# Kernel optimization log

Measured on AMD Instinct MI355X. Metric: run time of the kernel, lower is better.

Reference implementation:

```python
import jax, jax.numpy as jnp
import numpy as np

N, E, F, H, R, NB, G, C = 100000, 500000, 128, 64, 16, 30, 1000, 10


def setup_inputs() -> dict:
    key = jax.random.key(0)
    ks = jax.random.split(key, 12)
    s = 0.05
    x = jax.random.normal(ks[0], (N, F), jnp.float32)
    edge_index = jax.random.randint(ks[1], (2, E), 0, N, dtype=jnp.int32)
    edge_norm = jax.random.uniform(ks[2], (E,), jnp.float32)
    edge_type = jax.random.randint(ks[3], (E,), 0, R, dtype=jnp.int32)
    seq_lengths = jnp.full((G,), N // G, dtype=jnp.int32)  # 1000 graphs x 100 nodes
    return dict(
        x=x, edge_index=edge_index, edge_norm=edge_norm, edge_type=edge_type,
        seq_lengths=seq_lengths, avec=0,
        w1_rel=jax.random.normal(ks[4], (F, H), jnp.float32) * s,
        w1_root=jax.random.normal(ks[5], (F, H), jnp.float32) * s,
        b1=jnp.zeros((H,), jnp.float32),
        bases=jax.random.normal(ks[6], (NB, H, H), jnp.float32) * s,
        comp=jax.random.normal(ks[7], (R, NB), jnp.float32) * s,
        w2_root=jax.random.normal(ks[8], (H, H), jnp.float32) * s,
        b2=jnp.zeros((H,), jnp.float32),
        lin_w=jax.random.normal(ks[9], (2 * (F + H), H), jnp.float32) * s,
        lin_b=jnp.zeros((H,), jnp.float32),
        fc_w=jax.random.normal(ks[10], (H, C), jnp.float32) * s,
        fc_b=jnp.zeros((C,), jnp.float32),
    )


def reference(x, edge_index, edge_norm, edge_type, seq_lengths, avec,
              w1_rel, w1_root, b1, bases, comp, w2_root, b2,
              lin_w, lin_b, fc_w, fc_b):
    src, dst = edge_index[0], edge_index[1]

    # --- GraphConv (PyG): out_i = W_rel @ sum_{j->i} w_ji x_j + W_root x_i + b
    msg = x[src] * edge_norm[:, None]                       # [E, F]
    agg = jax.ops.segment_sum(msg, dst, num_segments=N)     # [N, F]
    h = agg @ w1_rel + x @ w1_root + b1                     # [N, H]

    # --- RGCNConv with basis decomposition, mean aggregation per relation
    W = jnp.einsum('rb,bio->rio', comp, bases)              # [R, H, H]
    hs = h[src]                                             # [E, H]
    out = h @ w2_root + b2                                  # root transform + bias
    for r in range(R):  # small fixed relation count
        m = (edge_type == r).astype(h.dtype)                # [E]
        s_r = jax.ops.segment_sum(hs * m[:, None], dst, num_segments=N)
        c_r = jax.ops.segment_sum(m, dst, num_segments=N)
        out = out + (s_r / jnp.maximum(c_r, 1.0)[:, None]) @ W[r]

    feats = jnp.concatenate([x, out], axis=-1)              # [N, F+H]

    # --- ragged per-graph sum & max pooling (replaces the Python loop)
    bounds = jnp.cumsum(seq_lengths)
    gid = jnp.searchsorted(bounds, jnp.arange(N), side='right')  # [N] graph ids
    gsum = jax.ops.segment_sum(feats, gid, num_segments=G)       # [G, F+H]
    gmax = jax.ops.segment_max(feats, gid, num_segments=G)       # [G, F+H]

    hidden = jax.nn.relu(jnp.concatenate([gsum, gmax], -1) @ lin_w + lin_b)
    # dropout is identity at inference
    logits = hidden @ fc_w + fc_b                           # [G, C]
    if avec:
        return logits
    return jax.nn.log_softmax(logits, -1)
```

## Files before the change

### kernel.cpp

```cpp
#include <hip/hip_runtime.h>
#include <hip/hip_bf16.h>

#define NN 100000
#define NE 500000
#define FD 128
#define HD 64
#define RR 16
#define NBASE 30
#define GG 1000
#define CC 10
#define NGROUP 6250
#define NBLK ((NE + 255) / 256)
#define NDBLK ((NN + 256) / 256)


typedef __attribute__((ext_vector_type(8))) short bf16x8;
typedef __attribute__((ext_vector_type(4))) float f32x4;

__device__ inline unsigned short f2b(float x) {
  __hip_bfloat16 b = __float2bfloat16(x);
  return *reinterpret_cast<unsigned short*>(&b);
}
__device__ inline float b2f(unsigned short u) {
  return __uint_as_float(((unsigned)u) << 16);
}
__device__ inline unsigned pk2(float a, float b) {
  return (unsigned)f2b(a) | ((unsigned)f2b(b) << 16);
}

__global__ void k_prep(const float* comp, const float* bases, const float* w_root,
                       const float* w_rel, const float* w2, unsigned short* Wt,
                       unsigned short* wcat2, unsigned short* w2t, int* hist2) {
  int bx = blockIdx.x;
  if (bx < 256) {
    int idx = bx * 256 + threadIdx.x;
    int r = idx >> 12, kj = idx & 4095;
    int k = kj >> 6, n = kj & 63;
    float acc = 0.0f;
    for (int b = 0; b < NBASE; ++b)
      acc += comp[r * NBASE + b] * bases[b * 4096 + kj];
    int sk = (k & 15) * 4 + (k >> 4);
    Wt[(r << 12) + n * 64 + sk] = f2b(acc);
  } else if (bx < 336) {
    int idx = (bx - 256) * 256 + threadIdx.x;
    if (idx < 16384) {
      int n = idx >> 7, k = idx & 127;
      float v = (n < 64) ? w_root[k * 64 + n] : w_rel[k * 64 + (n - 64)];
      int nt = n >> 4, m = n & 15;
      int s = k >> 5, q = (k >> 3) & 3, j = k & 7;
      wcat2[(((nt * 4 + s) * 64) + q * 16 + m) * 8 + j] = f2b(v);
    } else if (idx < 16384 + 4096) {
      int i2 = idx - 16384;
      int n = i2 >> 6, k = i2 & 63;
      int sk = (k & 15) * 4 + (k >> 4);
      w2t[n * 64 + sk] = f2b(w2[k * 64 + n]);
    }
  } else {
    int idx = (bx - 336) * 1024 + threadIdx.x * 4;
    if (idx < NN * RR)
      *reinterpret_cast<int4*>(hist2 + idx) = make_int4(0, 0, 0, 0);
  }
}

__global__ __launch_bounds__(256) void k_proj_mfma(const float* x, const unsigned short* wcat2,
                                                   const float* b1, unsigned short* hroot_bf,
                                                   unsigned short* xw_bf) {
  __shared__ unsigned short wsh[16384];
  int wv = threadIdx.x >> 6, l = threadIdx.x & 63, m = l & 15, q = l >> 4;
  int g = blockIdx.x * 4 + wv;
  int gc = (g < NGROUP) ? g : (NGROUP - 1);
  size_t n0 = (size_t)gc * 16;
  const float* xr = x + (n0 + m) * FD + q * 8;
  float4 xv[8];
#pragma unroll
  for (int s = 0; s < 4; ++s) {
    xv[2 * s] = *reinterpret_cast<const float4*>(xr + s * 32);
    xv[2 * s + 1] = *reinterpret_cast<const float4*>(xr + s * 32 + 4);
  }
  {
    const uint4* wsrc = reinterpret_cast<const uint4*>(wcat2);
    uint4* wdst = reinterpret_cast<uint4*>(wsh);
#pragma unroll
    for (int r = 0; r < 8; ++r)
      wdst[r * 256 + threadIdx.x] = wsrc[r * 256 + threadIdx.x];
  }
  __syncthreads();
  if (g >= NGROUP) return;
  bf16x8 afr[4];
#pragma unroll
  for (int s = 0; s < 4; ++s) {
    float4 xa = xv[2 * s], xb = xv[2 * s + 1];
    bf16x8 a;
    a[0] = (short)f2b(xa.x); a[1] = (short)f2b(xa.y);
    a[2] = (short)f2b(xa.z); a[3] = (short)f2b(xa.w);
    a[4] = (short)f2b(xb.x); a[5] = (short)f2b(xb.y);
    a[6] = (short)f2b(xb.z); a[7] = (short)f2b(xb.w);
    afr[s] = a;
  }
  f32x4 acc[8];
#pragma unroll
  for (int nt = 0; nt < 8; ++nt) acc[nt] = (f32x4){0, 0, 0, 0};
#pragma unroll
  for (int s = 0; s < 4; ++s) {
#pragma unroll
    for (int nt = 0; nt < 8; ++nt) {
      bf16x8 b = *reinterpret_cast<const bf16x8*>(wsh + (size_t)((nt * 4 + s) * 64 + l) * 8);
      acc[nt] = __builtin_amdgcn_mfma_f32_16x16x32_bf16(afr[s], b, acc[nt], 0, 0, 0);
    }
  }
  float bv[4];
#pragma unroll
  for (int nt = 0; nt < 4; ++nt) bv[nt] = b1[nt * 16 + m];
#pragma unroll
  for (int i = 0; i < 4; ++i) {
    size_t row = (n0 + q * 4 + i) * 64 + m * 4;
    uint2 oh, ox;
    oh.x = pk2(acc[0][i] + bv[0], acc[1][i] + bv[1]);
    oh.y = pk2(acc[2][i] + bv[2], acc[3][i] + bv[3]);
    ox.x = pk2(acc[4][i], acc[5][i]);
    ox.y = pk2(acc[6][i], acc[7][i]);
    *reinterpret_cast<uint2*>(hroot_bf + row) = oh;
    *reinterpret_cast<uint2*>(xw_bf + row) = ox;
  }
}

__global__ void k_hists(const int* ei, const int* etype, int* bch, int* hist2) {
  __shared__ int lh[RR];
  if (threadIdx.x < RR) lh[threadIdx.x] = 0;
  __syncthreads();
  int e = blockIdx.x * 256 + threadIdx.x;
  if (e < NE) {
    int t = etype[e];
    atomicAdd(&lh[t], 1);
    atomicAdd(&hist2[ei[NE + e] * RR + t], 1);
  }
  __syncthreads();
  if (threadIdx.x < RR) bch[blockIdx.x * RR + threadIdx.x] = lh[threadIdx.x];
}

__device__ inline int block_scan_incl(int v, int* ps, int t) {
  ps[t] = v;
  __syncthreads();
  for (int off = 1; off < 256; off <<= 1) {
    int u = (t >= off) ? ps[t - off] : 0;
    __syncthreads();
    ps[t] += u;
    __syncthreads();
  }
  return ps[t];
}

__device__ inline int dst_degree(const int* hist2, int dst) {
  const int4* hp = reinterpret_cast<const int4*>(hist2 + dst * RR);
  int4 a = hp[0], b = hp[1], c = hp[2], d = hp[3];
  return a.x + a.y + a.z + a.w + b.x + b.y + b.z + b.w +
         c.x + c.y + c.z + c.w + d.x + d.y + d.z + d.w;
}

__global__ void k_scanA(const int* hist2, int* bsum) {
  __shared__ int red[256];
  int t = threadIdx.x;
  int dst = blockIdx.x * 256 + t;
  red[t] = (dst < NN) ? dst_degree(hist2, dst) : 0;
  __syncthreads();
  for (int s = 128; s; s >>= 1) {
    if (t < s) red[t] += red[t + s];
    __syncthreads();
  }
  if (t == 0) bsum[blockIdx.x] = red[0];
}

__global__ void k_scanC(const int* hist2, const int* bsum, int* rowptr_d, int* ctr_d) {
  int t = threadIdx.x;
  int dst = blockIdx.x * 256 + t;
  int v = (dst < NN) ? dst_degree(hist2, dst) : 0;
  __shared__ int ps[256];
  int incl = block_scan_incl(v, ps, t);
  int ex = bsum[blockIdx.x] + incl - v;
  if (dst <= NN) { rowptr_d[dst] = ex; ctr_d[dst] = ex; }
}

__global__ void k_bscan(const int* bch, const int* seq, int* bsum, int* bbase,
                        int* offs, int* bounds) {
  __shared__ int part[16][17], chunkbase[16][17];
  __shared__ int colbase[16];
  __shared__ int ps[256];
  int t = threadIdx.x;
  {
    int i0 = t * 2, i1 = t * 2 + 1;
    int l0 = (i0 < NDBLK) ? bsum[i0] : 0;
    int l1 = (i1 < NDBLK) ? bsum[i1] : 0;
    int sa = l0 + l1;
    int incla = block_scan_incl(sa, ps, t);
    int run = incla - sa;
    if (i0 < NDBLK) bsum[i0] = run;
    run += l0;
    if (i1 < NDBLK) bsum[i1] = run;
  }
  __syncthreads();
  int ty = t & 15, ck = t >> 4;
  const int CH = (NBLK + 15) / 16;
  int b0 = ck * CH, b1 = min(b0 + CH, NBLK);
  int s = 0;
  for (int b = b0; b < b1; ++b) s += bch[b * 16 + ty];
  part[ck][ty] = s;
  __syncthreads();
  if (t < 16) {
    int run = 0;
    for (int c = 0; c < 16; ++c) { chunkbase[c][t] = run; run += part[c][t]; }
    colbase[t] = run;
  }
  __syncthreads();
  if (t == 0) {
    int run = 0;
    for (int r = 0; r < RR; ++r) { int v = colbase[r]; offs[r] = run; colbase[r] = run; run += v; }
    offs[RR] = run;
  }
  __syncthreads();
  {
    int run = colbase[ty] + chunkbase[ck][ty];
    for (int b = b0; b < b1; ++b) {
      int v = bch[b * 16 + ty];
      bbase[b * 16 + ty] = run;
      run += v;
    }
  }
  __syncthreads();
  int loc[4];
  int ss = 0;
  if (t < 250) {
    for (int i = 0; i < 4; ++i) { loc[i] = seq[t * 4 + i]; ss += loc[i]; }
  }
  int incl = block_scan_incl(ss, ps, t);
  int base = incl - ss;
  if (t < 250) {
    int run = base;
    for (int i = 0; i < 4; ++i) { run += loc[i]; bounds[t * 4 + i] = run; }
  }
}

__global__ void k_sort(const int* ei, const int* etype, const float* enorm,
                       const int* bbase, const int* hist2, int* ctr_d,
                       uint4* tse, uint2* esen) {
  __shared__ int lcnt[RR];
  if (threadIdx.x < RR) lcnt[threadIdx.x] = 0;
  __syncthreads();
  int e = blockIdx.x * 256 + threadIdx.x;
  if (e >= NE) return;
  int t = etype[e];
  int rank = atomicAdd(&lcnt[t], 1);
  int p = bbase[blockIdx.x * RR + t] + rank;
  int src = ei[e];
  int dst = ei[NE + e];
  int cnt = hist2[dst * RR + t];
  float inv = 1.0f / (float)max(cnt, 1);
  int pos = atomicAdd(&ctr_d[dst], 1);
  esen[pos] = make_uint2((unsigned)src, __float_as_uint(enorm[e]));
  tse[p] = make_uint4((unsigned)src, __float_as_uint(inv), (unsigned)pos, 0u);
}

__global__ __launch_bounds__(256) void k_gconv_seg(const int* rowptr_d, const uint2* esen,
    const unsigned short* xw_bf, const unsigned short* hroot_bf, unsigned short* h_bf) {
  int wv = threadIdx.x >> 6, l = threadIdx.x & 63;
  int c4 = l & 15, eq = l >> 4;
  int dst = blockIdx.x * 4 + wv;
  int lo = rowptr_d[dst];
  int hi = rowptr_d[dst + 1];
  float4 acc = {0.0f, 0.0f, 0.0f, 0.0f};
  for (int base0 = lo; base0 < hi; base0 += 64) {
    int n = min(64, hi - base0);
    int sv = 0;
    float nv = 0.0f;
    if (l < n) {
      uint2 se = esen[base0 + l];
      sv = (int)se.x;
      nv = __uint_as_float(se.y);
    }
    int k4max = (n + 3) >> 2;
    for (int k4 = 0; k4 < k4max; ++k4) {
      int eid = k4 * 4 + eq;
      int s = __shfl(sv, eid);
      float w = __shfl(nv, eid);
      if (eid < n) {
        uint2 v = *reinterpret_cast<const uint2*>(xw_bf + (size_t)s * 64 + c4 * 4);
        acc.x += b2f((unsigned short)(v.x & 0xffffu)) * w;
        acc.y += b2f((unsigned short)(v.x >> 16)) * w;
        acc.z += b2f((unsigned short)(v.y & 0xffffu)) * w;
        acc.w += b2f((unsigned short)(v.y >> 16)) * w;
      }
    }
  }
  acc.x += __shfl_xor(acc.x, 16); acc.y += __shfl_xor(acc.y, 16);
  acc.z += __shfl_xor(acc.z, 16); acc.w += __shfl_xor(acc.w, 16);
  acc.x += __shfl_xor(acc.x, 32); acc.y += __shfl_xor(acc.y, 32);
  acc.z += __shfl_xor(acc.z, 32); acc.w += __shfl_xor(acc.w, 32);
  if (l < 16) {
    uint2 hb = *reinterpret_cast<const uint2*>(hroot_bf + (size_t)dst * 64 + l * 4);
    acc.x += b2f((unsigned short)(hb.x & 0xffffu));
    acc.y += b2f((unsigned short)(hb.x >> 16));
    acc.z += b2f((unsigned short)(hb.y & 0xffffu));
    acc.w += b2f((unsigned short)(hb.y >> 16));
    uint2 o;
    o.x = pk2(acc.x, acc.y);
    o.y = pk2(acc.z, acc.w);
    *reinterpret_cast<uint2*>(h_bf + (size_t)dst * 64 + l * 4) = o;
  }
}

__global__ __launch_bounds__(256) void k_rgcn_y(const uint4* tse, const int* offs,
    const unsigned short* h_bf, const unsigned short* Wt, unsigned short* y_bf) {
  int r = blockIdx.x;
  int lo = offs[r], hi = offs[r + 1];
  int cnt = hi - lo;
  int wv = threadIdx.x >> 6;
  int l = threadIdx.x & 63;
  int m = l & 15, q = l >> 4;
  int ngroups = (cnt + 15) / 16;
  const unsigned short* Wr = Wt + (r << 12);
  bf16x8 bfr[2][4];
#pragma unroll
  for (int s = 0; s < 2; ++s)
#pragma unroll
    for (int nt = 0; nt < 4; ++nt)
      bfr[s][nt] = *reinterpret_cast<const bf16x8*>(Wr + (nt * 16 + m) * 64 + s * 32 + q * 8);

  for (int g = blockIdx.y * 4 + wv; g < ngroups; g += gridDim.y * 4) {
    int base = lo + g * 16;
    int ne = min(16, hi - base);
    int p = base + ((m < ne) ? m : 0);
    uint4 t4 = tse[p];
    int src = (int)t4.x;
    float inv = __uint_as_float(t4.y);
    int pos = (int)t4.z;
    f32x4 acc[4];
#pragma unroll
    for (int nt = 0; nt < 4; ++nt) acc[nt] = (f32x4){0, 0, 0, 0};
    const unsigned short* hrow = h_bf + (size_t)src * 64 + q * 8;
#pragma unroll
    for (int s = 0; s < 2; ++s) {
      bf16x8 afr = *reinterpret_cast<const bf16x8*>(hrow + s * 32);
#pragma unroll
      for (int nt = 0; nt < 4; ++nt)
        acc[nt] = __builtin_amdgcn_mfma_f32_16x16x32_bf16(afr, bfr[s][nt], acc[nt], 0, 0, 0);
    }
#pragma unroll
    for (int i = 0; i < 4; ++i) {
      int row = q * 4 + i;
      float ir = __shfl(inv, row);
      int pr = __shfl(pos, row);
      if (row < ne) {
        uint2 o;
        o.x = pk2(acc[0][i] * ir, acc[1][i] * ir);
        o.y = pk2(acc[2][i] * ir, acc[3][i] * ir);
        *reinterpret_cast<uint2*>(y_bf + (size_t)pr * 64 + m * 4) = o;
      }
    }
  }
}

__global__ __launch_bounds__(256) void k_out(const int* rowptr_d, const unsigned short* y_bf,
    const unsigned short* h_bf, const unsigned short* w2t, const float* b2, float* out) {
  __shared__ float ldsC[16][68];
  int wv = threadIdx.x >> 6, l = threadIdx.x & 63;
  int c4 = l & 15, eq = l >> 4;
  size_t d0 = (size_t)blockIdx.x * 16;
  for (int dd = 0; dd < 4; ++dd) {
    int dst = (int)d0 + wv * 4 + dd;
    int lo = rowptr_d[dst];
    int hi = rowptr_d[dst + 1];
    float4 acc = {0.0f, 0.0f, 0.0f, 0.0f};
    for (int row = lo + eq; row < hi; row += 4) {
      uint2 v = *reinterpret_cast<const uint2*>(y_bf + (size_t)row * 64 + c4 * 4);
      acc.x += b2f((unsigned short)(v.x & 0xffffu));
      acc.y += b2f((unsigned short)(v.x >> 16));
      acc.z += b2f((unsigned short)(v.y & 0xffffu));
      acc.w += b2f((unsigned short)(v.y >> 16));
    }
    acc.x += __shfl_xor(acc.x, 16); acc.y += __shfl_xor(acc.y, 16);
    acc.z += __shfl_xor(acc.z, 16); acc.w += __shfl_xor(acc.w, 16);
    acc.x += __shfl_xor(acc.x, 32); acc.y += __shfl_xor(acc.y, 32);
    acc.z += __shfl_xor(acc.z, 32); acc.w += __shfl_xor(acc.w, 32);
    if (l < 16)
      *reinterpret_cast<float4*>(&ldsC[wv * 4 + dd][l * 4]) = acc;
  }
  __syncthreads();
  int m = l & 15, q = l >> 4, nt = wv;
  float bb = b2[nt * 16 + m];
  f32x4 acc;
#pragma unroll
  for (int i = 0; i < 4; ++i) acc[i] = ldsC[q * 4 + i][m * 4 + nt] + bb;
#pragma unroll
  for (int s = 0; s < 2; ++s) {
    bf16x8 a = *reinterpret_cast<const bf16x8*>(h_bf + (d0 + m) * 64 + s * 32 + q * 8);
    bf16x8 b = *reinterpret_cast<const bf16x8*>(w2t + (nt * 16 + m) * 64 + s * 32 + q * 8);
    acc = __builtin_amdgcn_mfma_f32_16x16x32_bf16(a, b, acc, 0, 0, 0);
  }
#pragma unroll
  for (int i = 0; i < 4; ++i)
    out[(d0 + q * 4 + i) * 64 + nt * 16 + m] = acc[i];
}

__global__ __launch_bounds__(256) void k_head(const float* x, const float* outn,
    const int* bounds, const float* lin_w, const float* lin_b,
    const float* fc_w, const float* fc_b, float* dout) {
  __shared__ float4 psum[5][48], pmax[5][48];
  __shared__ float gsum[192], gmax[192];
  __shared__ float part[4][64];
  __shared__ float hid[HD], lg[CC], mred[2];
  int g = blockIdx.x, t = threadIdx.x;
  int lo = (g == 0) ? 0 : bounds[g - 1];
  int hi = bounds[g];
  int nn = hi - lo;
  if (t < 240) {
    int c4 = t % 48, ch = t / 48;
    int a = lo + (nn * ch) / 5, b = lo + (nn * (ch + 1)) / 5;
    float4 s = {0, 0, 0, 0};
    float4 mx = {-3.4e38f, -3.4e38f, -3.4e38f, -3.4e38f};
    const float* bp;
    int stride;
    if (c4 < 32) { bp = x + (size_t)a * FD + c4 * 4; stride = FD; }
    else         { bp = outn + (size_t)a * 64 + (c4 - 32) * 4; stride = 64; }
    int n = a;
    for (; n + 4 <= b; n += 4) {
      float4 v0 = *reinterpret_cast<const float4*>(bp);
      float4 v1 = *reinterpret_cast<const float4*>(bp + stride);
      float4 v2 = *reinterpret_cast<const float4*>(bp + 2 * stride);
      float4 v3 = *reinterpret_cast<const float4*>(bp + 3 * stride);
      bp += 4 * stride;
      s.x += v0.x + v1.x + v2.x + v3.x;
      s.y += v0.y + v1.y + v2.y + v3.y;
      s.z += v0.z + v1.z + v2.z + v3.z;
      s.w += v0.w + v1.w + v2.w + v3.w;
      mx.x = fmaxf(fmaxf(fmaxf(mx.x, v0.x), fmaxf(v1.x, v2.x)), v3.x);
      mx.y = fmaxf(fmaxf(fmaxf(mx.y, v0.y), fmaxf(v1.y, v2.y)), v3.y);
      mx.z = fmaxf(fmaxf(fmaxf(mx.z, v0.z), fmaxf(v1.z, v2.z)), v3.z);
      mx.w = fmaxf(fmaxf(fmaxf(mx.w, v0.w), fmaxf(v1.w, v2.w)), v3.w);
    }
    for (; n < b; ++n) {
      float4 v = *reinterpret_cast<const float4*>(bp);
      bp += stride;
      s.x += v.x; s.y += v.y; s.z += v.z; s.w += v.w;
      mx.x = fmaxf(mx.x, v.x); mx.y = fmaxf(mx.y, v.y);
      mx.z = fmaxf(mx.z, v.z); mx.w = fmaxf(mx.w, v.w);
    }
    psum[ch][c4] = s;
    pmax[ch][c4] = mx;
  }
  __syncthreads();
  if (t < 48) {
    float4 s = psum[0][t], m = pmax[0][t];
#pragma unroll
    for (int ch = 1; ch < 5; ++ch) {
      float4 ps = psum[ch][t], pm = pmax[ch][t];
      s.x += ps.x; s.y += ps.y; s.z += ps.z; s.w += ps.w;
      m.x = fmaxf(m.x, pm.x); m.y = fmaxf(m.y, pm.y);
      m.z = fmaxf(m.z, pm.z); m.w = fmaxf(m.w, pm.w);
    }
    gsum[t * 4 + 0] = s.x; gsum[t * 4 + 1] = s.y;
    gsum[t * 4 + 2] = s.z; gsum[t * 4 + 3] = s.w;
    gmax[t * 4 + 0] = m.x; gmax[t * 4 + 1] = m.y;
    gmax[t * 4 + 2] = m.z; gmax[t * 4 + 3] = m.w;
  }
  __syncthreads();
  {
    int o = t & 63, pp = t >> 6;
    float a = 0.0f;
    int k0 = pp * 96;
    for (int k = k0; k < k0 + 96; ++k) {
      float gv = (k < 192) ? gsum[k] : gmax[k - 192];
      a += gv * lin_w[k * 64 + o];
    }
    part[pp][o] = a;
  }
  __syncthreads();
  if (t < HD) {
    float a = lin_b[t] + part[0][t] + part[1][t] + part[2][t] + part[3][t];
    hid[t] = fmaxf(a, 0.0f);
  }
  __syncthreads();
  if (t < CC) {
    float a = fc_b[t];
    for (int k = 0; k < HD; ++k) a += hid[k] * fc_w[k * CC + t];
    lg[t] = a;
  }
  __syncthreads();
  if (t == 0) {
    float mm = lg[0];
#pragma unroll
    for (int i = 1; i < CC; ++i) mm = fmaxf(mm, lg[i]);
    float se = 0.0f;
#pragma unroll
    for (int i = 0; i < CC; ++i) se += __expf(lg[i] - mm);
    mred[0] = mm;
    mred[1] = __logf(se);
  }
  __syncthreads();
  if (t < CC) dout[g * CC + t] = lg[t] - mred[0] - mred[1];
}

extern "C" void kernel_launch(void* const* d_in, const int* in_sizes, int n_in,
                              void* d_out, int out_size, void* d_ws, size_t ws_size,
                              hipStream_t stream) {
  const float* x     = (const float*)d_in[0];
  const int* ei      = (const int*)d_in[1];
  const float* enorm = (const float*)d_in[2];
  const int* etype   = (const int*)d_in[3];
  const int* seq     = (const int*)d_in[4];
  const float* w1_rel  = (const float*)d_in[6];
  const float* w1_root = (const float*)d_in[7];
  const float* b1      = (const float*)d_in[8];
  const float* bases   = (const float*)d_in[9];
  const float* comp    = (const float*)d_in[10];
  const float* w2      = (const float*)d_in[11];
  const float* b2      = (const float*)d_in[12];
  const float* lin_w   = (const float*)d_in[13];
  const float* lin_b   = (const float*)d_in[14];
  const float* fc_w    = (const float*)d_in[15];
  const float* fc_b    = (const float*)d_in[16];
  float* dout = (float*)d_out;

  char* p = (char*)d_ws;
  unsigned short* hroot_bf = (unsigned short*)p; p += (size_t)NN * 64 * 2;
  unsigned short* xw_bf    = (unsigned short*)p; p += (size_t)NN * 64 * 2;
  float* out  = (float*)p;  p += (size_t)NN * 64 * 4;
  unsigned short* y_bf = (unsigned short*)p; p += (size_t)NE * 64 * 2;
  unsigned short* h_bf = (unsigned short*)p; p += (size_t)NN * 64 * 2;
  unsigned short* Wt   = (unsigned short*)p; p += (size_t)RR * 4096 * 2;
  unsigned short* wcat2 = (unsigned short*)p; p += (size_t)128 * 128 * 2;
  unsigned short* w2t  = (unsigned short*)p; p += (size_t)64 * 64 * 2;
  uint4* tse   = (uint4*)p; p += (size_t)NE * 16;
  uint2* esen  = (uint2*)p; p += (size_t)NE * 8;
  int* hist2   = (int*)p; p += (size_t)NN * RR * 4;
  int* rowptr_d = (int*)p; p += (size_t)(NDBLK * 256) * 4;
  int* bch     = (int*)p; p += (size_t)NBLK * RR * 4;
  int* bbase   = (int*)p; p += (size_t)NBLK * RR * 4;
  int* bsum    = (int*)p; p += (size_t)NGROUP * 4;
  int* offs    = (int*)p; p += 68;
  int* bounds  = (int*)p; p += (size_t)GG * 4;
  int* ctr_d   = (int*)out;

  const int ZBLK = (NN * RR + 1023) / 1024;
  hipLaunchKernelGGL(k_prep, dim3(336 + ZBLK), dim3(256), 0, stream,
                     comp, bases, w1_root, w1_rel, w2, Wt, wcat2, w2t, hist2);
  hipLaunchKernelGGL(k_proj_mfma, dim3((NGROUP + 3) / 4), dim3(256), 0, stream,
                     x, wcat2, b1, hroot_bf, xw_bf);
  hipLaunchKernelGGL(k_hists, dim3(NBLK), dim3(256), 0, stream, ei, etype, bch, hist2);
  hipLaunchKernelGGL(k_scanA, dim3(NDBLK), dim3(256), 0, stream, hist2, bsum);
  hipLaunchKernelGGL(k_bscan, dim3(1), dim3(256), 0, stream, bch, seq, bsum, bbase, offs, bounds);
  hipLaunchKernelGGL(k_scanC, dim3(NDBLK), dim3(256), 0, stream, hist2, bsum, rowptr_d, ctr_d);
  hipLaunchKernelGGL(k_sort, dim3(NBLK), dim3(256), 0, stream,
                     ei, etype, enorm, bbase, hist2, ctr_d, tse, esen);
  hipLaunchKernelGGL(k_gconv_seg, dim3(NN / 4), dim3(256), 0, stream,
                     rowptr_d, esen, xw_bf, hroot_bf, h_bf);
  hipLaunchKernelGGL(k_rgcn_y, dim3(RR, 128), dim3(256), 0, stream,
                     tse, offs, h_bf, Wt, y_bf);
  hipLaunchKernelGGL(k_out, dim3(NN / 16), dim3(256), 0, stream,
                     rowptr_d, y_bf, h_bf, w2t, b2, out);
  hipLaunchKernelGGL(k_head, dim3(GG), dim3(256), 0, stream, x, out, bounds,
                     lin_w, lin_b, fc_w, fc_b, dout);
}
```

Baseline: 331.1 us.

## Fuse per-graph sum/max pooling of RGCN output into k_out via atomics

k_out no longer writes the full per-node output; it reduces each 4-row fragment and atomically adds into per-graph sums and atomically maxes into order-preserving uint keys. k_head then only pools the x features and reads the pre-pooled RGCN part. This removes a large intermediate write and read, at the cost of global atomics and a binary search for graph ids in k_out. The zeroed workspace is extended to cover the new accumulators, and the counter buffer gets its own allocation.

```diff
diff --git a/kernel.cpp b/kernel.cpp
--- a/kernel.cpp
+++ b/kernel.cpp
@@ -12,6 +12,8 @@
 #define NGROUP 6250
 #define NBLK ((NE + 255) / 256)
 #define NDBLK ((NN + 256) / 256)
+#define TOTZ (NN * RR + GG * HD * 2)
+#define ZBLK ((TOTZ + 1023) / 1024)
 
 
 typedef __attribute__((ext_vector_type(8))) short bf16x8;
@@ -27,10 +29,18 @@
 __device__ inline unsigned pk2(float a, float b) {
   return (unsigned)f2b(a) | ((unsigned)f2b(b) << 16);
 }
+__device__ inline unsigned fkey(float f) {
+  unsigned b = __float_as_uint(f);
+  return (b & 0x80000000u) ? ~b : (b | 0x80000000u);
+}
+__device__ inline float fdec(unsigned k) {
+  unsigned b = (k & 0x80000000u) ? (k & 0x7FFFFFFFu) : ~k;
+  return __uint_as_float(b);
+}
 
 __global__ void k_prep(const float* comp, const float* bases, const float* w_root,
                        const float* w_rel, const float* w2, unsigned short* Wt,
-                       unsigned short* wcat2, unsigned short* w2t, int* hist2) {
+                       unsigned short* wcat2, unsigned short* w2t, int* zbase) {
   int bx = blockIdx.x;
   if (bx < 256) {
     int idx = bx * 256 + threadIdx.x;
@@ -57,8 +67,8 @@
     }
   } else {
     int idx = (bx - 336) * 1024 + threadIdx.x * 4;
-    if (idx < NN * RR)
-      *reinterpret_cast<int4*>(hist2 + idx) = make_int4(0, 0, 0, 0);
+    if (idx < TOTZ)
+      *reinterpret_cast<int4*>(zbase + idx) = make_int4(0, 0, 0, 0);
   }
 }
 
@@ -359,11 +369,22 @@
 }
 
 __global__ __launch_bounds__(256) void k_out(const int* rowptr_d, const unsigned short* y_bf,
-    const unsigned short* h_bf, const unsigned short* w2t, const float* b2, float* out) {
+    const unsigned short* h_bf, const unsigned short* w2t, const float* b2,
+    const int* bounds, float* gsum_out, unsigned* gmax_out) {
   __shared__ float ldsC[16][68];
+  __shared__ int gidv[16];
   int wv = threadIdx.x >> 6, l = threadIdx.x & 63;
   int c4 = l & 15, eq = l >> 4;
   size_t d0 = (size_t)blockIdx.x * 16;
+  if (threadIdx.x < 16) {
+    int dst = (int)d0 + threadIdx.x;
+    int lo2 = 0, hi2 = GG;
+    while (lo2 < hi2) {
+      int mid = (lo2 + hi2) >> 1;
+      if (bounds[mid] <= dst) lo2 = mid + 1; else hi2 = mid;
+    }
+    gidv[threadIdx.x] = lo2;
+  }
   for (int dd = 0; dd < 4; ++dd) {
     int dst = (int)d0 + wv * 4 + dd;
     int lo = rowptr_d[dst];
@@ -395,15 +416,27 @@
     bf16x8 b = *reinterpret_cast<const bf16x8*>(w2t + (nt * 16 + m) * 64 + s * 32 + q * 8);
     acc = __builtin_amdgcn_mfma_f32_16x16x32_bf16(a, b, acc, 0, 0, 0);
   }
-#pragma unroll
-  for (int i = 0; i < 4; ++i)
-    out[(d0 + q * 4 + i) * 64 + nt * 16 + m] = acc[i];
-}
-
-__global__ __launch_bounds__(256) void k_head(const float* x, const float* outn,
-    const int* bounds, const float* lin_w, const float* lin_b,
+  int c = nt * 16 + m;
+  int g0 = gidv[q * 4], g3 = gidv[q * 4 + 3];
+  if (g0 == g3) {
+    float ssum = acc[0] + acc[1] + acc[2] + acc[3];
+    float smax = fmaxf(fmaxf(acc[0], acc[1]), fmaxf(acc[2], acc[3]));
+    atomicAdd(&gsum_out[g0 * 64 + c], ssum);
+    atomicMax(&gmax_out[g0 * 64 + c], fkey(smax));
+  } else {
+#pragma unroll
+    for (int i = 0; i < 4; ++i) {
+      int gg = gidv[q * 4 + i];
+      atomicAdd(&gsum_out[gg * 64 + c], acc[i]);
+      atomicMax(&gmax_out[gg * 64 + c], fkey(acc[i]));
+    }
+  }
+}
+
+__global__ __launch_bounds__(256) void k_head(const float* x, const int* bounds,
+    const float* gsum_out, const unsigned* gmax_out, const float* lin_w, const float* lin_b,
     const float* fc_w, const float* fc_b, float* dout) {
-  __shared__ float4 psum[5][48], pmax[5][48];
+  __shared__ float4 psum[8][32], pmax[8][32];
   __shared__ float gsum[192], gmax[192];
   __shared__ float part[4][64];
   __shared__ float hid[HD], lg[CC], mred[2];
@@ -411,22 +444,19 @@
   int lo = (g == 0) ? 0 : bounds[g - 1];
   int hi = bounds[g];
   int nn = hi - lo;
-  if (t < 240) {
-    int c4 = t % 48, ch = t / 48;
-    int a = lo + (nn * ch) / 5, b = lo + (nn * (ch + 1)) / 5;
+  {
+    int c4 = t & 31, ch = t >> 5;
+    int a = lo + (nn * ch) / 8, b = lo + (nn * (ch + 1)) / 8;
     float4 s = {0, 0, 0, 0};
     float4 mx = {-3.4e38f, -3.4e38f, -3.4e38f, -3.4e38f};
-    const float* bp;
-    int stride;
-    if (c4 < 32) { bp = x + (size_t)a * FD + c4 * 4; stride = FD; }
-    else         { bp = outn + (size_t)a * 64 + (c4 - 32) * 4; stride = 64; }
+    const float* bp = x + (size_t)a * FD + c4 * 4;
     int n = a;
     for (; n + 4 <= b; n += 4) {
       float4 v0 = *reinterpret_cast<const float4*>(bp);
-      float4 v1 = *reinterpret_cast<const float4*>(bp + stride);
-      float4 v2 = *reinterpret_cast<const float4*>(bp + 2 * stride);
-      float4 v3 = *reinterpret_cast<const float4*>(bp + 3 * stride);
-      bp += 4 * stride;
+      float4 v1 = *reinterpret_cast<const float4*>(bp + FD);
+      float4 v2 = *reinterpret_cast<const float4*>(bp + 2 * FD);
+      float4 v3 = *reinterpret_cast<const float4*>(bp + 3 * FD);
+      bp += 4 * FD;
       s.x += v0.x + v1.x + v2.x + v3.x;
       s.y += v0.y + v1.y + v2.y + v3.y;
       s.z += v0.z + v1.z + v2.z + v3.z;
@@ -438,7 +468,7 @@
     }
     for (; n < b; ++n) {
       float4 v = *reinterpret_cast<const float4*>(bp);
-      bp += stride;
+      bp += FD;
       s.x += v.x; s.y += v.y; s.z += v.z; s.w += v.w;
       mx.x = fmaxf(mx.x, v.x); mx.y = fmaxf(mx.y, v.y);
       mx.z = fmaxf(mx.z, v.z); mx.w = fmaxf(mx.w, v.w);
@@ -447,10 +477,10 @@
     pmax[ch][c4] = mx;
   }
   __syncthreads();
-  if (t < 48) {
+  if (t < 32) {
     float4 s = psum[0][t], m = pmax[0][t];
 #pragma unroll
-    for (int ch = 1; ch < 5; ++ch) {
+    for (int ch = 1; ch < 8; ++ch) {
       float4 ps = psum[ch][t], pm = pmax[ch][t];
       s.x += ps.x; s.y += ps.y; s.z += ps.z; s.w += ps.w;
       m.x = fmaxf(m.x, pm.x); m.y = fmaxf(m.y, pm.y);
@@ -460,6 +490,10 @@
     gsum[t * 4 + 2] = s.z; gsum[t * 4 + 3] = s.w;
     gmax[t * 4 + 0] = m.x; gmax[t * 4 + 1] = m.y;
     gmax[t * 4 + 2] = m.z; gmax[t * 4 + 3] = m.w;
+  } else if (t < 96) {
+    int c = t - 32;
+    gsum[128 + c] = gsum_out[g * 64 + c];
+    gmax[128 + c] = fdec(gmax_out[g * 64 + c]);
   }
   __syncthreads();
   {
@@ -522,7 +556,6 @@
   char* p = (char*)d_ws;
   unsigned short* hroot_bf = (unsigned short*)p; p += (size_t)NN * 64 * 2;
   unsigned short* xw_bf    = (unsigned short*)p; p += (size_t)NN * 64 * 2;
-  float* out  = (float*)p;  p += (size_t)NN * 64 * 4;
   unsigned short* y_bf = (unsigned short*)p; p += (size_t)NE * 64 * 2;
   unsigned short* h_bf = (unsigned short*)p; p += (size_t)NN * 64 * 2;
   unsigned short* Wt   = (unsigned short*)p; p += (size_t)RR * 4096 * 2;
@@ -531,15 +564,16 @@
   uint4* tse   = (uint4*)p; p += (size_t)NE * 16;
   uint2* esen  = (uint2*)p; p += (size_t)NE * 8;
   int* hist2   = (int*)p; p += (size_t)NN * RR * 4;
+  float* gsum_out = (float*)p; p += (size_t)GG * 64 * 4;
+  unsigned* gmax_out = (unsigned*)p; p += (size_t)GG * 64 * 4;
   int* rowptr_d = (int*)p; p += (size_t)(NDBLK * 256) * 4;
+  int* ctr_d   = (int*)p; p += (size_t)(NDBLK * 256) * 4;
   int* bch     = (int*)p; p += (size_t)NBLK * RR * 4;
   int* bbase   = (int*)p; p += (size_t)NBLK * RR * 4;
   int* bsum    = (int*)p; p += (size_t)NGROUP * 4;
   int* offs    = (int*)p; p += 68;
   int* bounds  = (int*)p; p += (size_t)GG * 4;
-  int* ctr_d   = (int*)out;
-
-  const int ZBLK = (NN * RR + 1023) / 1024;
+
   hipLaunchKernelGGL(k_prep, dim3(336 + ZBLK), dim3(256), 0, stream,
                      comp, bases, w1_root, w1_rel, w2, Wt, wcat2, w2t, hist2);
   hipLaunchKernelGGL(k_proj_mfma, dim3((NGROUP + 3) / 4), dim3(256), 0, stream,
@@ -555,7 +589,7 @@
   hipLaunchKernelGGL(k_rgcn_y, dim3(RR, 128), dim3(256), 0, stream,
                      tse, offs, h_bf, Wt, y_bf);
   hipLaunchKernelGGL(k_out, dim3(NN / 16), dim3(256), 0, stream,
-                     rowptr_d, y_bf, h_bf, w2t, b2, out);
-  hipLaunchKernelGGL(k_head, dim3(GG), dim3(256), 0, stream, x, out, bounds,
-                     lin_w, lin_b, fc_w, fc_b, dout);
-}
+                     rowptr_d, y_bf, h_bf, w2t, b2, bounds, gsum_out, gmax_out);
+  hipLaunchKernelGGL(k_head, dim3(GG), dim3(256), 0, stream, x, bounds,
+                     gsum_out, gmax_out, lin_w, lin_b, fc_w, fc_b, dout);
+}
```

After: 350.4 us. 1.06x slower.
